# Kernel optimization log

Hardware: AMD Instinct MI355X
Metric: run time of the kernel (lower is better)

The kernel has to match this reference:

```python
import jax, jax.numpy as jnp
import numpy as np

B, T, C, H, L, V = 4, 1024, 1024, 16, 6, 32000
D = C // H
STD = 0.02


def setup_inputs() -> dict:
    key = jax.random.key(0)
    ks = jax.random.split(key, 12)
    return {
        "idx": jax.random.randint(ks[0], (B, T), 0, V),
        "tok_emb": jax.random.normal(ks[1], (V, C), jnp.float32) * STD,
        "pos_emb": jax.random.normal(ks[2], (T, C), jnp.float32) * STD,
        "qkv_w": jax.random.normal(ks[3], (L, C, 3 * C), jnp.float32) * STD,
        "attn_out_w": jax.random.normal(ks[4], (L, C, C), jnp.float32) * STD,
        "attn_out_b": jnp.zeros((L, C), jnp.float32),
        "fc1_w": jax.random.normal(ks[5], (L, C, 4 * C), jnp.float32) * STD,
        "fc1_b": jnp.zeros((L, 4 * C), jnp.float32),
        "fc2_w": jax.random.normal(ks[6], (L, 4 * C, C), jnp.float32) * STD,
        "fc2_b": jnp.zeros((L, C), jnp.float32),
        "ln1_w": jnp.ones((L, C), jnp.float32),
        "ln1_b": jnp.zeros((L, C), jnp.float32),
        "ln2_w": jnp.ones((L, C), jnp.float32),
        "ln2_b": jnp.zeros((L, C), jnp.float32),
        "lnf_w": jnp.ones((C,), jnp.float32),
        "lnf_b": jnp.zeros((C,), jnp.float32),
        "head_w": jax.random.normal(ks[7], (C, V), jnp.float32) * STD,
    }


def layernorm(x, w, b, eps=1e-5):
    mu = jnp.mean(x, axis=-1, keepdims=True)
    var = jnp.var(x, axis=-1, keepdims=True)
    return (x - mu) * jax.lax.rsqrt(var + eps) * w + b


def attention(x, qkv_w, out_w, out_b, causal_mask):
    # x: (B,T,C)
    qkv = jnp.einsum("btc,cf->btf", x, qkv_w)  # (B,T,3C)
    q, k, v = jnp.split(qkv, 3, axis=-1)
    q = q.reshape(B, T, H, D).transpose(0, 2, 1, 3)  # (B,H,T,D)
    k = k.reshape(B, T, H, D).transpose(0, 2, 1, 3)
    v = v.reshape(B, T, H, D).transpose(0, 2, 1, 3)
    scores = jnp.einsum("bhqd,bhkd->bhqk", q, k) / np.sqrt(D).astype(np.float32)
    scores = jnp.where(causal_mask, scores, -jnp.inf)
    w = jax.nn.softmax(scores, axis=-1)
    out = jnp.einsum("bhqk,bhkd->bhqd", w, v)  # (B,H,T,D)
    out = out.transpose(0, 2, 1, 3).reshape(B, T, C)
    return jnp.einsum("btc,cd->btd", out, out_w) + out_b


def reference(idx, tok_emb, pos_emb, qkv_w, attn_out_w, attn_out_b,
              fc1_w, fc1_b, fc2_w, fc2_b, ln1_w, ln1_b, ln2_w, ln2_b,
              lnf_w, lnf_b, head_w):
    causal_mask = jnp.tril(jnp.ones((T, T), dtype=bool))[None, None]  # (1,1,T,T)
    x = tok_emb[idx] + pos_emb[jnp.arange(T)][None]  # (B,T,C)
    for l in range(L):
        h = layernorm(x, ln1_w[l], ln1_b[l])
        x = x + attention(h, qkv_w[l], attn_out_w[l], attn_out_b[l], causal_mask)
        h = layernorm(x, ln2_w[l], ln2_b[l])
        h = jax.nn.relu(jnp.einsum("btc,cf->btf", h, fc1_w[l]) + fc1_b[l])
        x = x + jnp.einsum("btf,fc->btc", h, fc2_w[l]) + fc2_b[l]
    x = layernorm(x, lnf_w, lnf_b)
    logits = jnp.einsum("btc,cv->btv", x, head_w)  # (B,T,V)
    return logits
```

## Files before the change

### kernel.cpp

```cpp
#include <hip/hip_runtime.h>
#include <cstdint>
#include <cstddef>

typedef __bf16 bf16_t;
typedef __bf16 bf16x8 __attribute__((ext_vector_type(8)));
typedef float f32x4 __attribute__((ext_vector_type(4)));
typedef int i32x4 __attribute__((ext_vector_type(4)));

#define B_ 4
#define T_ 1024
#define C_ 1024
#define H_ 16
#define L_ 6
#define V_ 32000
#define M_ (B_ * T_)

__global__ __launch_bounds__(256) void k_embed(const int* __restrict__ idx,
                                               const float* __restrict__ tok,
                                               const float* __restrict__ pos,
                                               float* __restrict__ x) {
  int row = blockIdx.x;
  int t = row & (T_ - 1);
  int id = idx[row];
  int c = threadIdx.x * 4;
  f32x4 a = *(const f32x4*)(tok + (size_t)id * C_ + c);
  f32x4 p = *(const f32x4*)(pos + (size_t)t * C_ + c);
  *(f32x4*)(x + (size_t)row * C_ + c) = a + p;
}

__global__ __launch_bounds__(256) void k_ln(const float* __restrict__ x,
                                            const float* __restrict__ w,
                                            const float* __restrict__ b,
                                            bf16_t* __restrict__ out) {
  __shared__ float red[8];
  int row = blockIdx.x;
  int tid = threadIdx.x;
  const float* xr = x + (size_t)row * C_;
  f32x4 v = *(const f32x4*)(xr + tid * 4);
  float s = v[0] + v[1] + v[2] + v[3];
  float q = v[0] * v[0] + v[1] * v[1] + v[2] * v[2] + v[3] * v[3];
#pragma unroll
  for (int off = 32; off; off >>= 1) {
    s += __shfl_xor(s, off);
    q += __shfl_xor(q, off);
  }
  int wid = tid >> 6;
  if ((tid & 63) == 0) { red[wid * 2] = s; red[wid * 2 + 1] = q; }
  __syncthreads();
  s = red[0] + red[2] + red[4] + red[6];
  q = red[1] + red[3] + red[5] + red[7];
  float mu = s * (1.f / C_);
  float var = q * (1.f / C_) - mu * mu;
  float rstd = rsqrtf(var + 1e-5f);
  f32x4 wv = *(const f32x4*)(w + tid * 4);
  f32x4 bv = *(const f32x4*)(b + tid * 4);
  bf16_t* o = out + (size_t)row * C_ + tid * 4;
#pragma unroll
  for (int j = 0; j < 4; j++) o[j] = (bf16_t)((v[j] - mu) * rstd * wv[j] + bv[j]);
}

__global__ __launch_bounds__(256) void k_transpose_bf16(const float* __restrict__ in,
                                                        bf16_t* __restrict__ out,
                                                        int K, int N) {
  __shared__ float tile[32][33];
  int n0 = blockIdx.x * 32, k0 = blockIdx.y * 32;
  int tid = threadIdx.x;
  int cr = tid >> 5, cc = tid & 31;
#pragma unroll
  for (int it = 0; it < 4; it++) {
    int r = it * 8 + cr;
    tile[r][cc] = in[(size_t)(k0 + r) * N + n0 + cc];
  }
  __syncthreads();
#pragma unroll
  for (int it = 0; it < 4; it++) {
    int r = it * 8 + cr;
    out[(size_t)(n0 + r) * K + k0 + cc] = (bf16_t)tile[cc][r];
  }
}

__global__ __launch_bounds__(256) void k_reshape_qk(const bf16_t* __restrict__ qkv,
                                                    bf16_t* __restrict__ qh,
                                                    bf16_t* __restrict__ kh) {
  int g = blockIdx.x * 256 + threadIdx.x;
  int d = g & 63;
  int t = (g >> 6) & (T_ - 1);
  int h = (g >> 16) & (H_ - 1);
  int b = g >> 20;
  size_t src = ((size_t)(b * T_ + t)) * (3 * C_) + h * 64 + d;
  qh[g] = (bf16_t)((float)qkv[src] * 0.125f);
  kh[g] = qkv[src + C_];
}

__global__ __launch_bounds__(256) void k_vtrans(const bf16_t* __restrict__ qkv,
                                                bf16_t* __restrict__ vT) {
  __shared__ bf16_t tile[64][65];
  int bh = blockIdx.x;
  int t0 = blockIdx.y * 64;
  int tid = threadIdx.x;
  int c = tid & 63, rr = tid >> 6;
  int b = bh >> 4, h = bh & (H_ - 1);
  const bf16_t* src = qkv + ((size_t)(b * T_ + t0)) * (3 * C_) + 2 * C_ + h * 64;
#pragma unroll
  for (int it = 0; it < 16; it++) {
    int r = it * 4 + rr;
    tile[r][c] = src[(size_t)r * (3 * C_) + c];
  }
  __syncthreads();
  bf16_t* dst = vT + (size_t)bh * 64 * T_ + t0;
#pragma unroll
  for (int it = 0; it < 16; it++) {
    int dr = it * 4 + rr;
    dst[(size_t)dr * T_ + c] = tile[c][dr];
  }
}

__global__ __launch_bounds__(256) void k_attn(const bf16_t* __restrict__ qh,
                                              const bf16_t* __restrict__ kh,
                                              const bf16_t* __restrict__ vT,
                                              bf16_t* __restrict__ outb) {
  __shared__ bf16_t p_lds[4][16 * 32];
  int tid = threadIdx.x, lane = tid & 63, wid = tid >> 6;
  int bh = blockIdx.x;
  int b = bh >> 4, h = bh & (H_ - 1);
  int qbase = blockIdx.y * 64 + wid * 16;
  const bf16_t* qp = qh + ((size_t)bh * T_ + qbase) * 64;
  const bf16_t* kp = kh + (size_t)bh * T_ * 64;
  const bf16_t* vp = vT + (size_t)bh * 64 * T_;
  int r = lane & 15, g = lane >> 4;

  bf16x8 qf0 = *(const bf16x8*)(qp + r * 64 + g * 8);
  bf16x8 qf1 = *(const bf16x8*)(qp + r * 64 + 32 + g * 8);

  f32x4 o[4];
  float m[4], l[4];
#pragma unroll
  for (int j = 0; j < 4; j++) { m[j] = -1e30f; l[j] = 0.f; o[j] = (f32x4){0.f, 0.f, 0.f, 0.f}; }

  int kv_end = qbase + 16;
  for (int jb = 0; jb < kv_end; jb += 32) {
    f32x4 s0 = (f32x4){0.f, 0.f, 0.f, 0.f};
    f32x4 s1 = (f32x4){0.f, 0.f, 0.f, 0.f};
    const bf16_t* kb0 = kp + (size_t)(jb + r) * 64 + g * 8;
    const bf16_t* kb1 = kb0 + 16 * 64;
    s0 = __builtin_amdgcn_mfma_f32_16x16x32_bf16(qf0, *(const bf16x8*)(kb0), s0, 0, 0, 0);
    s0 = __builtin_amdgcn_mfma_f32_16x16x32_bf16(qf1, *(const bf16x8*)(kb0 + 32), s0, 0, 0, 0);
    s1 = __builtin_amdgcn_mfma_f32_16x16x32_bf16(qf0, *(const bf16x8*)(kb1), s1, 0, 0, 0);
    s1 = __builtin_amdgcn_mfma_f32_16x16x32_bf16(qf1, *(const bf16x8*)(kb1 + 32), s1, 0, 0, 0);

    float p0[4], p1[4], fac[4];
#pragma unroll
    for (int j = 0; j < 4; j++) {
      int rowg = qbase + g * 4 + j;
      float v0 = s0[j], v1 = s1[j];
      if (jb + r > rowg) v0 = -1e30f;
      if (jb + 16 + r > rowg) v1 = -1e30f;
      float t = fmaxf(v0, v1);
      t = fmaxf(t, __shfl_xor(t, 1));
      t = fmaxf(t, __shfl_xor(t, 2));
      t = fmaxf(t, __shfl_xor(t, 4));
      t = fmaxf(t, __shfl_xor(t, 8));
      float nm = fmaxf(m[j], t);
      p0[j] = __expf(v0 - nm);
      p1[j] = __expf(v1 - nm);
      float f = __expf(m[j] - nm);
      float ts = p0[j] + p1[j];
      ts += __shfl_xor(ts, 1);
      ts += __shfl_xor(ts, 2);
      ts += __shfl_xor(ts, 4);
      ts += __shfl_xor(ts, 8);
      l[j] = l[j] * f + ts;
      m[j] = nm;
      fac[j] = f;
    }
    f32x4 fv = (f32x4){fac[0], fac[1], fac[2], fac[3]};
#pragma unroll
    for (int d = 0; d < 4; d++) o[d] *= fv;

    bf16_t* pl = p_lds[wid];
#pragma unroll
    for (int j = 0; j < 4; j++) {
      pl[(g * 4 + j) * 32 + r] = (bf16_t)p0[j];
      pl[(g * 4 + j) * 32 + 16 + r] = (bf16_t)p1[j];
    }
    bf16x8 pa = *(const bf16x8*)(pl + r * 32 + g * 8);
#pragma unroll
    for (int d = 0; d < 4; d++) {
      const bf16_t* vf = vp + (size_t)(d * 16 + r) * T_ + jb + g * 8;
      o[d] = __builtin_amdgcn_mfma_f32_16x16x32_bf16(pa, *(const bf16x8*)(vf), o[d], 0, 0, 0);
    }
  }

#pragma unroll
  for (int d = 0; d < 4; d++) {
#pragma unroll
    for (int j = 0; j < 4; j++) {
      float val = o[d][j] / l[j];
      outb[((size_t)(b * T_ + qbase + g * 4 + j)) * C_ + h * 64 + d * 16 + r] = (bf16_t)val;
    }
  }
}

__device__ __forceinline__ void gld_lds16(const bf16_t* g, bf16_t* l) {
  __builtin_amdgcn_global_load_lds((const __attribute__((address_space(1))) void*)g,
                                   (__attribute__((address_space(3))) void*)l, 16, 0, 0);
}
__device__ __forceinline__ bf16x8 lds_rd128(uint32_t addr) {
  i32x4 d;
  asm volatile("ds_read_b128 %0, %1" : "=v"(d) : "v"(addr));
  return __builtin_bit_cast(bf16x8, d);
}
#define BAR_() __builtin_amdgcn_s_barrier()
#define SCHED0_() __builtin_amdgcn_sched_barrier(0)
#define WLGN_(n)                                                           \
  do {                                                                     \
    asm volatile("s_waitcnt lgkmcnt(" #n ")" ::: "memory");                \
    SCHED0_();                                                             \
  } while (0)

template <int OUTBF, int HASB, int HASRELU, int HASRES>
__global__ __launch_bounds__(256) void k_gemm(const bf16_t* __restrict__ A,
                                              const bf16_t* __restrict__ Bt,
                                              const float* __restrict__ bias,
                                              const float* resid,
                                              void* Cout, int M, int N, int K) {
  __shared__ bf16_t As[2][128 * 32];
  __shared__ bf16_t Bs[2][128 * 32];
  int tid = threadIdx.x;
  int lane = tid & 63, wid = tid >> 6;
  size_t rowBase = (size_t)blockIdx.y * 128;
  size_t colBase = (size_t)blockIdx.x * 128;

  const bf16_t* gA = A + (rowBase + (tid >> 2)) * (size_t)K + (tid & 3) * 8;
  const bf16_t* gB = Bt + (colBase + (tid >> 2)) * (size_t)K + (tid & 3) * 8;
  const size_t gStep64 = (size_t)64 * K;

  f32x4 acc[4][4];
#pragma unroll
  for (int i = 0; i < 4; i++)
#pragma unroll
    for (int j = 0; j < 4; j++) acc[i][j] = (f32x4){0.f, 0.f, 0.f, 0.f};

  int NK = K >> 5;
  {
    bf16_t* la = &As[0][0] + wid * 512;
    bf16_t* lb = &Bs[0][0] + wid * 512;
    gld_lds16(gA, la);            gld_lds16(gA + gStep64, la + 2048);
    gld_lds16(gB, lb);            gld_lds16(gB + gStep64, lb + 2048);
  }

  int wr = (wid >> 1) * 64, wc = (wid & 1) * 64;
  int r15 = lane & 15, g4 = lane >> 4;

  for (int kt = 0; kt < NK; kt++) {
    int buf = kt & 1;
    __syncthreads();
    if (kt + 1 < NK) {
      const bf16_t* ga = gA + (size_t)(kt + 1) * 32;
      const bf16_t* gb = gB + (size_t)(kt + 1) * 32;
      bf16_t* la = &As[buf ^ 1][0] + wid * 512;
      bf16_t* lb = &Bs[buf ^ 1][0] + wid * 512;
      gld_lds16(ga, la);          gld_lds16(ga + gStep64, la + 2048);
      gld_lds16(gb, lb);          gld_lds16(gb + gStep64, lb + 2048);
    }
    const bf16_t* as = &As[buf][0] + (wr + r15) * 32 + g4 * 8;
    const bf16_t* bs = &Bs[buf][0] + (wc + r15) * 32 + g4 * 8;
    bf16x8 af[4], bfr[4];
#pragma unroll
    for (int i = 0; i < 4; i++) af[i] = *(const bf16x8*)(as + i * 16 * 32);
#pragma unroll
    for (int i = 0; i < 4; i++) bfr[i] = *(const bf16x8*)(bs + i * 16 * 32);
#pragma unroll
    for (int i = 0; i < 4; i++)
#pragma unroll
      for (int j = 0; j < 4; j++)
        acc[i][j] = __builtin_amdgcn_mfma_f32_16x16x32_bf16(af[i], bfr[j], acc[i][j], 0, 0, 0);
  }

#pragma unroll
  for (int i = 0; i < 4; i++) {
    size_t row0 = rowBase + wr + i * 16 + g4 * 4;
#pragma unroll
    for (int j = 0; j < 4; j++) {
      size_t col = colBase + wc + j * 16 + r15;
      float bi = HASB ? bias[col] : 0.f;
#pragma unroll
      for (int q = 0; q < 4; q++) {
        size_t row = row0 + q;
        float v = acc[i][j][q] + bi;
        if (HASRELU) v = fmaxf(v, 0.f);
        if (HASRES) v += resid[row * (size_t)N + col];
        if (OUTBF)
          ((bf16_t*)Cout)[row * (size_t)N + col] = (bf16_t)v;
        else
          ((float*)Cout)[row * (size_t)N + col] = v;
      }
    }
  }
}

#define STAGE_(q, tk, bufv)                                                           \
  do {                                                                                \
    const bf16_t* _ga = A + (size_t)(rowBase + (q)*64 + srow) * (size_t)K +           \
                        (size_t)(tk)*64 + scol;                                       \
    const bf16_t* _gb = Bt + (size_t)(colBase + (q)*64 + srow) * (size_t)K +          \
                        (size_t)(tk)*64 + scol;                                       \
    gld_lds16(_ga, AsF + (bufv)*16384 + (q)*4096 + w * 512);                          \
    gld_lds16(_gb, BsF + (bufv)*16384 + (q)*4096 + w * 512);                          \
  } while (0)

#define RDS_(aset, bset, kk, bufv)                                                    \
  do {                                                                                \
    uint32_t _off = (kk) ? offK1 : offK0;                                             \
    uint32_t _ab = aRd + (uint32_t)(bufv)*32768u + _off;                              \
    uint32_t _bb = bRd + (uint32_t)(bufv)*32768u + _off;                              \
    _Pragma("unroll") for (int _m = 0; _m < 8; _m++)                                  \
        aset[_m] = lds_rd128(_ab + _m * 2048);                                        \
    _Pragma("unroll") for (int _n = 0; _n < 4; _n++)                                  \
        bset[_n] = lds_rd128(_bb + _n * 2048);                                        \
  } while (0)

#define MFH_(aset, bset)                                                              \
  do {                                                                                \
    __builtin_amdgcn_s_setprio(1);                                                    \
    _Pragma("unroll") for (int _m = 0; _m < 8; _m++)                                  \
        _Pragma("unroll") for (int _n = 0; _n < 4; _n++)                              \
            acc[_m][_n] = __builtin_amdgcn_mfma_f32_16x16x32_bf16(                    \
                aset[_m], bset[_n], acc[_m][_n], 0, 0, 0);                            \
    __builtin_amdgcn_s_setprio(0);                                                    \
  } while (0)

template <int OUTBF, int HASB, int HASRELU, int HASRES>
__global__ __launch_bounds__(512, 2) void k_gemm256(const bf16_t* __restrict__ A,
                                                    const bf16_t* __restrict__ Bt,
                                                    const float* __restrict__ bias,
                                                    const float* resid,
                                                    void* Cout, int M, int N, int K) {
  __shared__ bf16_t As[2][256][64];
  __shared__ bf16_t Bs[2][256][64];
  bf16_t* AsF = &As[0][0][0];
  bf16_t* BsF = &Bs[0][0][0];
  const uint32_t asb = (uint32_t)(uintptr_t)AsF;
  const uint32_t bsb = (uint32_t)(uintptr_t)BsF;

  int tid = threadIdx.x, lane = tid & 63, w = tid >> 6;
  int wr = w >> 2, wc = w & 3;
  int r15 = lane & 15, g4 = lane >> 4;

  int nwg = (int)gridDim.x;
  int bid = (int)blockIdx.x;
  int xcd = bid & 7, loc = bid >> 3;
  int q8 = nwg >> 3, r8 = nwg & 7;
  int swz = (xcd < r8) ? xcd * (q8 + 1) + loc : r8 * (q8 + 1) + (xcd - r8) * q8 + loc;
  int nY = M >> 8;
  int by = swz % nY, bx = swz / nY;
  int rowBase = by * 256, colBase = bx * 256;

  int srow = w * 8 + (lane >> 3);
  int scol = ((lane & 7) ^ (lane >> 3)) * 8;

  uint32_t xm = (uint32_t)((r15 & 7) << 4);
  uint32_t offK0 = ((uint32_t)(g4 * 16)) ^ xm;
  uint32_t offK1 = ((uint32_t)(g4 * 16 + 64)) ^ xm;
  uint32_t aRd = asb + (uint32_t)((wr * 128 + r15) * 128);
  uint32_t bRd = bsb + (uint32_t)((wc * 64 + r15) * 128);

  f32x4 acc[8][4];
#pragma unroll
  for (int i = 0; i < 8; i++)
#pragma unroll
    for (int j = 0; j < 4; j++) acc[i][j] = (f32x4){0.f, 0.f, 0.f, 0.f};

  bf16x8 a0[8], a1[8], b0[4], b1[4];

#pragma unroll
  for (int q = 0; q < 4; q++) STAGE_(q, 0, 0);
  asm volatile("s_waitcnt vmcnt(0)" ::: "memory");
  BAR_();
  RDS_(a0, b0, 0, 0);

  int NT = K >> 6;
  for (int kt = 0; kt < NT; ++kt) {
    int buf = kt & 1;
    bool pf = (kt + 1 < NT);
    if (pf) {
#pragma unroll
      for (int q = 0; q < 4; q++) STAGE_(q, kt + 1, buf ^ 1);
    }
    RDS_(a1, b1, 1, buf);
    WLGN_(12);
    MFH_(a0, b0);
    if (pf) {
      asm volatile("s_waitcnt vmcnt(0)" ::: "memory");
      BAR_();
      RDS_(a0, b0, 0, buf ^ 1);
      WLGN_(12);
    } else {
      WLGN_(0);
    }
    MFH_(a1, b1);
    BAR_();
  }

#pragma unroll
  for (int m = 0; m < 8; m++) {
    size_t row0 = (size_t)rowBase + wr * 128 + m * 16 + g4 * 4;
#pragma unroll
    for (int n = 0; n < 4; n++) {
      size_t col = (size_t)colBase + wc * 64 + n * 16 + r15;
      float bi = HASB ? bias[col] : 0.f;
#pragma unroll
      for (int qq = 0; qq < 4; qq++) {
        size_t row = row0 + qq;
        float v = acc[m][n][qq] + bi;
        if (HASRELU) v = fmaxf(v, 0.f);
        if (HASRES) v += resid[row * (size_t)N + col];
        if (OUTBF)
          ((bf16_t*)Cout)[row * (size_t)N + col] = (bf16_t)v;
        else
          ((float*)Cout)[row * (size_t)N + col] = v;
      }
    }
  }
}

extern "C" void kernel_launch(void* const* d_in, const int* in_sizes, int n_in,
                              void* d_out, int out_size, void* d_ws, size_t ws_size,
                              hipStream_t stream) {
  (void)in_sizes; (void)n_in; (void)out_size; (void)ws_size;
  const int* idx = (const int*)d_in[0];
  const float* tok_emb = (const float*)d_in[1];
  const float* pos_emb = (const float*)d_in[2];
  const float* qkv_w = (const float*)d_in[3];
  const float* attn_out_w = (const float*)d_in[4];
  const float* attn_out_b = (const float*)d_in[5];
  const float* fc1_w = (const float*)d_in[6];
  const float* fc1_b = (const float*)d_in[7];
  const float* fc2_w = (const float*)d_in[8];
  const float* fc2_b = (const float*)d_in[9];
  const float* ln1_w = (const float*)d_in[10];
  const float* ln1_b = (const float*)d_in[11];
  const float* ln2_w = (const float*)d_in[12];
  const float* ln2_b = (const float*)d_in[13];
  const float* lnf_w = (const float*)d_in[14];
  const float* lnf_b = (const float*)d_in[15];
  const float* head_w = (const float*)d_in[16];
  float* out = (float*)d_out;

  char* wsp = (char*)d_ws;
  auto alloc = [&](size_t bytes) {
    char* p = wsp;
    wsp += (bytes + 255) & ~(size_t)255;
    return p;
  };
  float* x      = (float*)alloc((size_t)M_ * C_ * 4);
  bf16_t* hbuf  = (bf16_t*)alloc((size_t)M_ * C_ * 2);
  bf16_t* qkvb  = (bf16_t*)alloc((size_t)M_ * 3 * C_ * 2);
  bf16_t* qhb   = (bf16_t*)alloc((size_t)M_ * C_ * 2);
  bf16_t* khb   = (bf16_t*)alloc((size_t)M_ * C_ * 2);
  bf16_t* vTb   = (bf16_t*)alloc((size_t)M_ * C_ * 2);
  bf16_t* attnb = (bf16_t*)alloc((size_t)M_ * C_ * 2);
  bf16_t* midb  = (bf16_t*)alloc((size_t)M_ * 4 * C_ * 2);
  bf16_t* qkvwT = (bf16_t*)alloc((size_t)3 * C_ * C_ * 2);
  bf16_t* owT   = (bf16_t*)alloc((size_t)C_ * C_ * 2);
  bf16_t* fc1wT = (bf16_t*)alloc((size_t)4 * C_ * C_ * 2);
  bf16_t* fc2wT = (bf16_t*)alloc((size_t)4 * C_ * C_ * 2);
  bf16_t* headwT= (bf16_t*)alloc((size_t)C_ * V_ * 2);

  k_embed<<<M_, 256, 0, stream>>>(idx, tok_emb, pos_emb, x);
  k_transpose_bf16<<<dim3(V_ / 32, C_ / 32), 256, 0, stream>>>(head_w, headwT, C_, V_);

  for (int l = 0; l < L_; l++) {
    k_transpose_bf16<<<dim3(3 * C_ / 32, C_ / 32), 256, 0, stream>>>(
        qkv_w + (size_t)l * C_ * 3 * C_, qkvwT, C_, 3 * C_);
    k_transpose_bf16<<<dim3(C_ / 32, C_ / 32), 256, 0, stream>>>(
        attn_out_w + (size_t)l * C_ * C_, owT, C_, C_);
    k_transpose_bf16<<<dim3(4 * C_ / 32, C_ / 32), 256, 0, stream>>>(
        fc1_w + (size_t)l * C_ * 4 * C_, fc1wT, C_, 4 * C_);
    k_transpose_bf16<<<dim3(C_ / 32, 4 * C_ / 32), 256, 0, stream>>>(
        fc2_w + (size_t)l * 4 * C_ * C_, fc2wT, 4 * C_, C_);

    k_ln<<<M_, 256, 0, stream>>>(x, ln1_w + l * C_, ln1_b + l * C_, hbuf);
    k_gemm256<1, 0, 0, 0><<<dim3((3 * C_ / 256) * (M_ / 256)), 512, 0, stream>>>(
        hbuf, qkvwT, nullptr, nullptr, qkvb, M_, 3 * C_, C_);
    k_reshape_qk<<<(M_ * C_) / 256, 256, 0, stream>>>(qkvb, qhb, khb);
    k_vtrans<<<dim3(B_ * H_, T_ / 64), 256, 0, stream>>>(qkvb, vTb);
    k_attn<<<dim3(B_ * H_, T_ / 64), 256, 0, stream>>>(qhb, khb, vTb, attnb);
    k_gemm<0, 1, 0, 1><<<dim3(C_ / 128, M_ / 128), 256, 0, stream>>>(
        attnb, owT, attn_out_b + l * C_, x, x, M_, C_, C_);

    k_ln<<<M_, 256, 0, stream>>>(x, ln2_w + l * C_, ln2_b + l * C_, hbuf);
    k_gemm256<1, 1, 1, 0><<<dim3((4 * C_ / 256) * (M_ / 256)), 512, 0, stream>>>(
        hbuf, fc1wT, fc1_b + (size_t)l * 4 * C_, nullptr, midb, M_, 4 * C_, C_);
    k_gemm<0, 1, 0, 1><<<dim3(C_ / 128, M_ / 128), 256, 0, stream>>>(
        midb, fc2wT, fc2_b + l * C_, x, x, M_, C_, 4 * C_);
  }

  k_ln<<<M_, 256, 0, stream>>>(x, lnf_w, lnf_b, hbuf);
  k_gemm256<0, 0, 0, 0><<<dim3((V_ / 256) * (M_ / 256)), 512, 0, stream>>>(
      hbuf, headwT, nullptr, nullptr, out, M_, V_, C_);
}
```

Before: 2.340 ms.

## Add XCD-aware block swizzle, XOR LDS swizzle, and simplify big-GEMM pipeline

In the 128x128 GEMM, workgroup IDs are remapped so that blocks landing on the same XCD (round-robin by ID mod 8) cover contiguous column-major tiles, which is meant to improve L2 reuse. An XOR swizzle is applied to the global-to-LDS write column and to the matching LDS reads, to cut LDS bank conflicts. In the 256-tile kernel, the cross-iteration prefetch of the first half of the LDS fragments is replaced by reading both halves at the top of each iteration, with a single barrier at the end. This removes a mid-iteration barrier but gives up some overlap between LDS reads and MFMA work.

```diff
diff --git a/kernel.cpp b/kernel.cpp
--- a/kernel.cpp
+++ b/kernel.cpp
@@ -228,11 +228,19 @@
   __shared__ bf16_t Bs[2][128 * 32];
   int tid = threadIdx.x;
   int lane = tid & 63, wid = tid >> 6;
-  size_t rowBase = (size_t)blockIdx.y * 128;
-  size_t colBase = (size_t)blockIdx.x * 128;
-
-  const bf16_t* gA = A + (rowBase + (tid >> 2)) * (size_t)K + (tid & 3) * 8;
-  const bf16_t* gB = Bt + (colBase + (tid >> 2)) * (size_t)K + (tid & 3) * 8;
+
+  int nwg = (int)(gridDim.x * gridDim.y);
+  int bid = (int)(blockIdx.y * gridDim.x + blockIdx.x);
+  int xcd = bid & 7, loc = bid >> 3;
+  int q8 = nwg >> 3, r8 = nwg & 7;
+  int swz = (xcd < r8) ? xcd * (q8 + 1) + loc : r8 * (q8 + 1) + (xcd - r8) * q8 + loc;
+  int nY = M >> 7;
+  size_t rowBase = (size_t)(swz % nY) * 128;
+  size_t colBase = (size_t)(swz / nY) * 128;
+
+  int scolE = (((tid & 3) ^ ((tid >> 2) & 3) ^ ((tid >> 4) & 3)) * 8);
+  const bf16_t* gA = A + (rowBase + (tid >> 2)) * (size_t)K + scolE;
+  const bf16_t* gB = Bt + (colBase + (tid >> 2)) * (size_t)K + scolE;
   const size_t gStep64 = (size_t)64 * K;
 
   f32x4 acc[4][4];
@@ -251,6 +259,7 @@
 
   int wr = (wid >> 1) * 64, wc = (wid & 1) * 64;
   int r15 = lane & 15, g4 = lane >> 4;
+  uint32_t roff = (uint32_t)((g4 * 8) ^ (((r15 & 3) ^ ((r15 >> 2) & 3)) << 3));
 
   for (int kt = 0; kt < NK; kt++) {
     int buf = kt & 1;
@@ -263,13 +272,15 @@
       gld_lds16(ga, la);          gld_lds16(ga + gStep64, la + 2048);
       gld_lds16(gb, lb);          gld_lds16(gb + gStep64, lb + 2048);
     }
-    const bf16_t* as = &As[buf][0] + (wr + r15) * 32 + g4 * 8;
-    const bf16_t* bs = &Bs[buf][0] + (wc + r15) * 32 + g4 * 8;
+    const bf16_t* asb = &As[buf][0];
+    const bf16_t* bsb = &Bs[buf][0];
     bf16x8 af[4], bfr[4];
 #pragma unroll
-    for (int i = 0; i < 4; i++) af[i] = *(const bf16x8*)(as + i * 16 * 32);
-#pragma unroll
-    for (int i = 0; i < 4; i++) bfr[i] = *(const bf16x8*)(bs + i * 16 * 32);
+    for (int i = 0; i < 4; i++)
+      af[i] = *(const bf16x8*)(asb + (wr + r15 + i * 16) * 32 + roff);
+#pragma unroll
+    for (int i = 0; i < 4; i++)
+      bfr[i] = *(const bf16x8*)(bsb + (wc + r15 + i * 16) * 32 + roff);
 #pragma unroll
     for (int i = 0; i < 4; i++)
 #pragma unroll
@@ -377,7 +388,6 @@
   for (int q = 0; q < 4; q++) STAGE_(q, 0, 0);
   asm volatile("s_waitcnt vmcnt(0)" ::: "memory");
   BAR_();
-  RDS_(a0, b0, 0, 0);
 
   int NT = K >> 6;
   for (int kt = 0; kt < NT; ++kt) {
@@ -387,18 +397,13 @@
 #pragma unroll
       for (int q = 0; q < 4; q++) STAGE_(q, kt + 1, buf ^ 1);
     }
+    RDS_(a0, b0, 0, buf);
     RDS_(a1, b1, 1, buf);
     WLGN_(12);
     MFH_(a0, b0);
-    if (pf) {
-      asm volatile("s_waitcnt vmcnt(0)" ::: "memory");
-      BAR_();
-      RDS_(a0, b0, 0, buf ^ 1);
-      WLGN_(12);
-    } else {
-      WLGN_(0);
-    }
+    WLGN_(0);
     MFH_(a1, b1);
+    asm volatile("s_waitcnt vmcnt(0)" ::: "memory");
     BAR_();
   }
 
```

New measurement: 2.248 ms. 3.9% less time.
